# Kernel optimization log

Hardware: AMD Instinct MI355X
Metric: run time of the kernel (lower is better)

Reference implementation:

```python
import jax, jax.numpy as jnp
import numpy as np

LN_EPS = 1e-5


def setup_inputs() -> dict:
    key = jax.random.key(0)
    ks = jax.random.split(key, 6)
    N_NODES, N_EDGES, D, H, E = 100000, 20000, 128, 64, 1000000
    node_feat = jax.random.normal(ks[0], (N_NODES, D), dtype=jnp.float32)
    edge_feat = jax.random.normal(ks[1], (N_EDGES, D), dtype=jnp.float32)
    gamma = jnp.ones((2 * D,), dtype=jnp.float32)
    beta = jnp.zeros((2 * D,), dtype=jnp.float32)
    # xavier_uniform-like init
    lim1 = float(np.sqrt(6.0 / (2 * D + H)))
    lim2 = float(np.sqrt(6.0 / (H + 1)))
    W1 = jax.random.uniform(ks[2], (2 * D, H), minval=-lim1, maxval=lim1, dtype=jnp.float32)
    b1 = jnp.zeros((H,), dtype=jnp.float32)
    W2 = jax.random.uniform(ks[3], (H, 1), minval=-lim2, maxval=lim2, dtype=jnp.float32)
    b2 = jnp.zeros((1,), dtype=jnp.float32)
    node_idx = jax.random.randint(ks[4], (E,), 0, N_NODES, dtype=jnp.int64 if jax.config.read('jax_enable_x64') else jnp.int32)
    edge_idx = jax.random.randint(ks[5], (E,), 0, N_EDGES, dtype=node_idx.dtype)
    return {"node_feat": node_feat, "edge_feat": edge_feat, "gamma": gamma, "beta": beta,
            "W1": W1, "b1": b1, "W2": W2, "b2": b2,
            "node_idx": node_idx, "edge_idx": edge_idx}


def reference(node_feat, edge_feat, gamma, beta, W1, b1, W2, b2, node_idx, edge_idx):
    # Gather incidence-pair embeddings: [E, D] each
    emb_node = node_feat[node_idx]
    emb_edge = edge_feat[edge_idx]
    # combined: [E, 2D], order = [edge, node] as in torch.cat([emb_edge, emb_node], 1)
    combined = jnp.concatenate([emb_edge, emb_node], axis=1)
    # LayerNorm over last dim
    mu = jnp.mean(combined, axis=-1, keepdims=True)
    var = jnp.var(combined, axis=-1, keepdims=True)
    xn = (combined - mu) * jax.lax.rsqrt(var + LN_EPS) * gamma + beta
    # MLP: Linear -> ReLU -> Linear, output [E, 1]
    h = jax.nn.relu(xn @ W1 + b1)
    return h @ W2 + b2
```

## Files before the change

kernel.cpp:

```cpp
#include <hip/hip_runtime.h>

#define LN_EPS 1e-5f
#define DD 128
#define TWO_D 256
#define HH 64

typedef unsigned int uint;
typedef __attribute__((ext_vector_type(8))) short short8v;
typedef __attribute__((ext_vector_type(4))) float f32x4;

__device__ __forceinline__ unsigned short f2bf(float f) {
    uint u = __float_as_uint(f);
    u += 0x7FFFu + ((u >> 16) & 1u);
    return (unsigned short)(u >> 16);
}
__device__ __forceinline__ float bf2f(unsigned short h) {
    return __uint_as_float(((uint)h) << 16);
}

__global__ __launch_bounds__(256) void k_fused(
    const float* __restrict__ node_feat, int n_nodes, int nbN,
    const float* __restrict__ edge_feat, int n_edges,
    const float* __restrict__ gamma, const float* __restrict__ beta,
    const float* __restrict__ W1, const float* __restrict__ b1,
    unsigned short* __restrict__ node_pt, float2* __restrict__ node_sums,
    unsigned short* __restrict__ edge_pt, float2* __restrict__ edge_sums,
    float* __restrict__ GB) {
    int bid = blockIdx.x;
    int tid = threadIdx.x;

    if (bid == 0) {
        if (tid < 128) {
            int h = tid & 63;
            bool isB = tid >= 64;
            float acc = isB ? b1[h] : 0.f;
            const float* coef = isB ? beta : gamma;
#pragma unroll 8
            for (int d = 0; d < TWO_D; ++d)
                acc = fmaf(coef[d], W1[d * HH + h], acc);
            GB[tid] = acc;
        }
        return;
    }

    const float* feat;
    int nrows, gofs, rbase0;
    unsigned short* pt;
    float2* sums;
    if (bid <= nbN) {
        feat = node_feat; nrows = n_nodes; gofs = 128;
        rbase0 = (bid - 1) * 128; pt = node_pt; sums = node_sums;
    } else {
        feat = edge_feat; nrows = n_edges; gofs = 0;
        rbase0 = (bid - 1 - nbN) * 128; pt = edge_pt; sums = edge_sums;
    }

    __shared__ __align__(16) char lds[49152];

    {
        int l = tid & 63;
        int w = tid >> 6;
#pragma unroll
        for (int ci = 0; ci < 4; ++ci) {
            int combo = ci * 4 + w;
            int ks = combo & 3;
            int ht = combo >> 2;
            int kbase = gofs + ks * 32 + (l >> 4) * 8;
            int h = ht * 16 + (l & 15);
            unsigned short vals[8];
#pragma unroll
            for (int j = 0; j < 8; ++j)
                vals[j] = f2bf(gamma[kbase + j] * W1[(size_t)(kbase + j) * HH + h]);
            short8v v;
#pragma unroll
            for (int j = 0; j < 8; ++j) v[j] = (short)vals[j];
            *(short8v*)(lds + 32768 + combo * 1024 + l * 16) = v;
        }
    }

    {
        float4 tmp[16];
#pragma unroll
        for (int u = 0; u < 16; ++u) {
            int F4 = u * 256 + tid;
            int r = F4 >> 5;
            int rg = rbase0 + r;
            rg = rg < nrows ? rg : (nrows - 1);
            int c4 = (F4 & 31) * 4;
            tmp[u] = *(const float4*)&feat[(size_t)rg * DD + c4];
        }
#pragma unroll
        for (int u = 0; u < 16; ++u) {
            int F4 = u * 256 + tid;
            int r = F4 >> 5;
            int c4 = (F4 & 31) * 4;
            uint2 wv;
            wv.x = (uint)f2bf(tmp[u].x) | ((uint)f2bf(tmp[u].y) << 16);
            wv.y = (uint)f2bf(tmp[u].z) | ((uint)f2bf(tmp[u].w) << 16);
            int byte = (r * 256 + c4 * 2) ^ ((r & 7) << 4);
            *(uint2*)(lds + byte) = wv;
        }
    }

    __syncthreads();

    int w = tid >> 6;
    int lane = tid & 63;
    f32x4 acc[2][4];
#pragma unroll
    for (int i = 0; i < 2; ++i)
#pragma unroll
        for (int j = 0; j < 4; ++j) acc[i][j] = (f32x4){0.f, 0.f, 0.f, 0.f};

    int arow_lo = lane & 15;
    int akofs = (lane >> 4) * 8;
#pragma unroll
    for (int ks = 0; ks < 4; ++ks) {
        int kk = ks * 32 + akofs;
        int rr0 = (2 * w) * 16 + arow_lo;
        int rr1 = rr0 + 16;
        short8v a0 = *(const short8v*)(lds + ((rr0 * 256 + kk * 2) ^ ((rr0 & 7) << 4)));
        short8v a1 = *(const short8v*)(lds + ((rr1 * 256 + kk * 2) ^ ((rr1 & 7) << 4)));
#pragma unroll
        for (int ht = 0; ht < 4; ++ht) {
            short8v b = *(const short8v*)(lds + 32768 + (ht * 4 + ks) * 1024 + lane * 16);
            acc[0][ht] = __builtin_amdgcn_mfma_f32_16x16x32_bf16(a0, b, acc[0][ht], 0, 0, 0);
            acc[1][ht] = __builtin_amdgcn_mfma_f32_16x16x32_bf16(a1, b, acc[1][ht], 0, 0, 0);
        }
    }

    {
        int row = tid >> 1, half = tid & 1;
        float s = 0.f, q = 0.f;
#pragma unroll
        for (int i = 0; i < 8; ++i) {
            int byte = (row * 256 + half * 128 + i * 16) ^ ((row & 7) << 4);
            short8v v = *(const short8v*)(lds + byte);
#pragma unroll
            for (int j = 0; j < 8; ++j) {
                float x = bf2f((unsigned short)v[j]);
                s += x;
                q = fmaf(x, x, q);
            }
        }
        s += __shfl_xor(s, 1);
        q += __shfl_xor(q, 1);
        if (half == 0 && rbase0 + row < nrows) sums[rbase0 + row] = make_float2(s, q);
    }

    __syncthreads();

    {
        unsigned short* ob = (unsigned short*)(lds + 32768);
        int colh = lane & 15;
        int rquad = lane >> 4;
#pragma unroll
        for (int rt = 0; rt < 2; ++rt)
#pragma unroll
            for (int ht = 0; ht < 4; ++ht)
#pragma unroll
                for (int reg = 0; reg < 4; ++reg) {
                    int r = (2 * w + rt) * 16 + rquad * 4 + reg;
                    int h = ht * 16 + colh;
                    ob[r * 64 + h] = f2bf(acc[rt][ht][reg]);
                }
        int row = tid >> 1;
        if (rbase0 + row < nrows) {
#pragma unroll
            for (int i = 0; i < 4; ++i) {
                short8v v = *(const short8v*)(lds + 32768 + tid * 64 + i * 16);
                *(short8v*)&pt[(size_t)rbase0 * HH + tid * 32 + i * 8] = v;
            }
        }
    }
}

__global__ __launch_bounds__(256) void k_pairs(const int* __restrict__ node_idx,
                                               const int* __restrict__ edge_idx,
                                               const unsigned short* __restrict__ node_pt,
                                               const unsigned short* __restrict__ edge_pt,
                                               const float2* __restrict__ node_sums,
                                               const float2* __restrict__ edge_sums,
                                               const float* __restrict__ Gv,
                                               const float* __restrict__ Bv,
                                               const float* __restrict__ W2,
                                               const float* __restrict__ b2,
                                               float* __restrict__ out, int E) {
    int gtid = blockIdx.x * 256 + threadIdx.x;
    int l = gtid & 7;
    int grp = gtid >> 3;
    int ngrps = (gridDim.x * 256) >> 3;

    float G8[8], B8[8], W8[8];
#pragma unroll
    for (int j = 0; j < 8; ++j) {
        G8[j] = Gv[l * 8 + j];
        B8[j] = Bv[l * 8 + j];
        W8[j] = W2[l * 8 + j];
    }
    float b2v = b2[0];

#pragma unroll 2
    for (int p = grp; p < E; p += ngrps) {
        int ni = node_idx[p];
        int ei = edge_idx[p];
        uint4 ue = *(const uint4*)&edge_pt[(size_t)ei * HH + l * 8];
        uint4 un = *(const uint4*)&node_pt[(size_t)ni * HH + l * 8];
        float2 se = edge_sums[ei];
        float2 sn = node_sums[ni];

        float S = se.x + sn.x;
        float Q = se.y + sn.y;
        float mu = S * (1.f / TWO_D);
        float var = fmaf(Q, 1.f / TWO_D, -mu * mu);
        float rstd = rsqrtf(var + LN_EPS);
        float nmu = -mu;

        uint ue_[4] = {ue.x, ue.y, ue.z, ue.w};
        uint un_[4] = {un.x, un.y, un.z, un.w};
        float acc = 0.f;
#pragma unroll
        for (int j = 0; j < 4; ++j) {
            float pe0 = __uint_as_float(ue_[j] << 16);
            float pe1 = __uint_as_float(ue_[j] & 0xFFFF0000u);
            float pn0 = __uint_as_float(un_[j] << 16);
            float pn1 = __uint_as_float(un_[j] & 0xFFFF0000u);
            float t0 = fmaf(nmu, G8[2 * j], pe0 + pn0);
            float v0 = fmaf(rstd, t0, B8[2 * j]);
            v0 = fmaxf(v0, 0.f);
            acc = fmaf(v0, W8[2 * j], acc);
            float t1 = fmaf(nmu, G8[2 * j + 1], pe1 + pn1);
            float v1 = fmaf(rstd, t1, B8[2 * j + 1]);
            v1 = fmaxf(v1, 0.f);
            acc = fmaf(v1, W8[2 * j + 1], acc);
        }

        acc += __shfl_xor(acc, 1);
        acc += __shfl_xor(acc, 2);
        acc += __shfl_xor(acc, 4);

        if (l == 0) out[p] = acc + b2v;
    }
}

extern "C" void kernel_launch(void* const* d_in, const int* in_sizes, int n_in,
                              void* d_out, int out_size, void* d_ws, size_t ws_size,
                              hipStream_t stream) {
    const float* node_feat = (const float*)d_in[0];
    const float* edge_feat = (const float*)d_in[1];
    const float* gamma = (const float*)d_in[2];
    const float* beta = (const float*)d_in[3];
    const float* W1 = (const float*)d_in[4];
    const float* b1 = (const float*)d_in[5];
    const float* W2 = (const float*)d_in[6];
    const float* b2 = (const float*)d_in[7];
    const int* node_idx = (const int*)d_in[8];
    const int* edge_idx = (const int*)d_in[9];

    int n_nodes = in_sizes[0] / DD;
    int n_edges = in_sizes[1] / DD;
    int E = in_sizes[8];

    float* ws = (float*)d_ws;
    float* GB = ws;
    float2* node_sums = (float2*)(ws + 128);
    float2* edge_sums = node_sums + n_nodes;

    size_t off = 128 + 2 * (size_t)n_nodes + 2 * (size_t)n_edges;
    off = (off + 31) & ~(size_t)31;
    unsigned short* node_pt = (unsigned short*)(ws + off);
    unsigned short* edge_pt = node_pt + (size_t)n_nodes * HH;

    int nbN = (n_nodes + 127) / 128;
    int nbE = (n_edges + 127) / 128;

    k_fused<<<1 + nbN + nbE, 256, 0, stream>>>(node_feat, n_nodes, nbN,
                                               edge_feat, n_edges,
                                               gamma, beta, W1, b1,
                                               node_pt, node_sums,
                                               edge_pt, edge_sums, GB);
    k_pairs<<<2048, 256, 0, stream>>>(node_idx, edge_idx, node_pt, edge_pt,
                                      node_sums, edge_sums, GB, GB + 64, W2, b2,
                                      (float*)d_out, E);
}
```

Measured before the change: 55.08 us.

## Bin incidence pairs by node index range to improve gather locality

Adds a pre-pass that counts and scatters (node, edge, position) records into 8 buckets keyed by node-index range, then a pair kernel processes each bucket so concurrent blocks gather from a narrower slice of node projections. The aim is to raise L2 hit rate for the random bf16 node row gathers. It adds two extra launches, extra index read/write traffic and scattered output stores, and falls back to the old kernel when index ranges or workspace size don't fit the packing.

```diff
diff --git a/kernel.cpp b/kernel.cpp
--- a/kernel.cpp
+++ b/kernel.cpp
@@ -172,6 +172,115 @@
                 *(short8v*)&pt[(size_t)rbase0 * HH + tid * 32 + i * 8] = v;
             }
         }
+    }
+}
+
+__global__ void k_zero8(uint* gcnt) { gcnt[threadIdx.x] = 0; }
+
+__global__ __launch_bounds__(256) void k_bin(const int* __restrict__ node_idx,
+                                             const int* __restrict__ edge_idx,
+                                             int E, float scale, uint* __restrict__ gcnt,
+                                             uint2* __restrict__ binned, int Ecap) {
+    __shared__ uint lc[8];
+    __shared__ uint lofs[8];
+    int tid = threadIdx.x;
+    if (tid < 8) lc[tid] = 0;
+    __syncthreads();
+    int per = (E + (int)gridDim.x - 1) / (int)gridDim.x;
+    int s = blockIdx.x * per;
+    int e = s + per < E ? s + per : E;
+    for (int p = s + tid; p < e; p += 256) {
+        int b = (int)((float)node_idx[p] * scale);
+        b = b < 7 ? b : 7;
+        atomicAdd(&lc[b], 1u);
+    }
+    __syncthreads();
+    if (tid < 8) lofs[tid] = atomicAdd(&gcnt[tid], lc[tid]);
+    __syncthreads();
+    for (int p = s + tid; p < e; p += 256) {
+        int ni = node_idx[p];
+        int ei = edge_idx[p];
+        int b = (int)((float)ni * scale);
+        b = b < 7 ? b : 7;
+        uint pos = atomicAdd(&lofs[b], 1u);
+        binned[(size_t)b * Ecap + pos] = make_uint2((uint)ni | ((uint)ei << 17), (uint)p);
+    }
+}
+
+__global__ __launch_bounds__(256) void k_pairs_b(const uint2* __restrict__ binned, int Ecap,
+                                                 const uint* __restrict__ gcnt,
+                                                 const unsigned short* __restrict__ node_pt,
+                                                 const unsigned short* __restrict__ edge_pt,
+                                                 const float2* __restrict__ node_sums,
+                                                 const float2* __restrict__ edge_sums,
+                                                 const float* __restrict__ Gv,
+                                                 const float* __restrict__ Bv,
+                                                 const float* __restrict__ W2,
+                                                 const float* __restrict__ b2,
+                                                 float* __restrict__ out) {
+    int bucket = blockIdx.x & 7;
+    int nchunk = (int)gridDim.x >> 3;
+    int chunk = blockIdx.x >> 3;
+    uint sz = gcnt[bucket];
+    uint per = (sz + nchunk - 1) / nchunk;
+    uint beg = chunk * per;
+    uint end = beg + per < sz ? beg + per : sz;
+    const uint2* bb = binned + (size_t)bucket * Ecap;
+
+    int tid = threadIdx.x;
+    int l = tid & 7;
+    int grp = tid >> 3;
+
+    float G8[8], B8[8], W8[8];
+#pragma unroll
+    for (int j = 0; j < 8; ++j) {
+        G8[j] = Gv[l * 8 + j];
+        B8[j] = Bv[l * 8 + j];
+        W8[j] = W2[l * 8 + j];
+    }
+    float b2v = b2[0];
+
+#pragma unroll 2
+    for (uint i = beg + grp; i < end; i += 32) {
+        uint2 rec = bb[i];
+        uint ni = rec.x & 0x1FFFFu;
+        uint ei = rec.x >> 17;
+        uint4 ue = *(const uint4*)&edge_pt[(size_t)ei * HH + l * 8];
+        uint4 un = *(const uint4*)&node_pt[(size_t)ni * HH + l * 8];
+        float2 se = edge_sums[ei];
+        float2 sn = node_sums[ni];
+
+        float S = se.x + sn.x;
+        float Q = se.y + sn.y;
+        float mu = S * (1.f / TWO_D);
+        float var = fmaf(Q, 1.f / TWO_D, -mu * mu);
+        float rstd = rsqrtf(var + LN_EPS);
+        float nmu = -mu;
+
+        uint ue_[4] = {ue.x, ue.y, ue.z, ue.w};
+        uint un_[4] = {un.x, un.y, un.z, un.w};
+        float acc = 0.f;
+#pragma unroll
+        for (int j = 0; j < 4; ++j) {
+            float pe0 = __uint_as_float(ue_[j] << 16);
+            float pe1 = __uint_as_float(ue_[j] & 0xFFFF0000u);
+            float pn0 = __uint_as_float(un_[j] << 16);
+            float pn1 = __uint_as_float(un_[j] & 0xFFFF0000u);
+            float t0 = fmaf(nmu, G8[2 * j], pe0 + pn0);
+            float v0 = fmaf(rstd, t0, B8[2 * j]);
+            v0 = fmaxf(v0, 0.f);
+            acc = fmaf(v0, W8[2 * j], acc);
+            float t1 = fmaf(nmu, G8[2 * j + 1], pe1 + pn1);
+            float v1 = fmaf(rstd, t1, B8[2 * j + 1]);
+            v1 = fmaxf(v1, 0.f);
+            acc = fmaf(v1, W8[2 * j + 1], acc);
+        }
+
+        acc += __shfl_xor(acc, 1);
+        acc += __shfl_xor(acc, 2);
+        acc += __shfl_xor(acc, 4);
+
+        if (l == 0) out[rec.y] = acc + b2v;
     }
 }
 
@@ -261,25 +370,43 @@
     int n_edges = in_sizes[1] / DD;
     int E = in_sizes[8];
 
-    float* ws = (float*)d_ws;
-    float* GB = ws;
-    float2* node_sums = (float2*)(ws + 128);
-    float2* edge_sums = node_sums + n_nodes;
-
-    size_t off = 128 + 2 * (size_t)n_nodes + 2 * (size_t)n_edges;
-    off = (off + 31) & ~(size_t)31;
-    unsigned short* node_pt = (unsigned short*)(ws + off);
-    unsigned short* edge_pt = node_pt + (size_t)n_nodes * HH;
+    char* wsb = (char*)d_ws;
+    size_t o = 0;
+    float* GB = (float*)(wsb + o); o += 512;
+    float2* node_sums = (float2*)(wsb + o); o += (size_t)n_nodes * 8;
+    float2* edge_sums = (float2*)(wsb + o); o += (size_t)n_edges * 8;
+    o = (o + 127) & ~(size_t)127;
+    unsigned short* node_pt = (unsigned short*)(wsb + o); o += (size_t)n_nodes * HH * 2;
+    unsigned short* edge_pt = (unsigned short*)(wsb + o); o += (size_t)n_edges * HH * 2;
+    o = (o + 127) & ~(size_t)127;
+    uint* gcnt = (uint*)(wsb + o); o += 128;
+    uint2* binned = (uint2*)(wsb + o);
+    size_t need = o + (size_t)8 * (size_t)E * sizeof(uint2);
+
+    bool can_bin = (n_nodes <= (1 << 17)) && (n_edges <= (1 << 15)) && (ws_size >= need);
 
     int nbN = (n_nodes + 127) / 128;
     int nbE = (n_edges + 127) / 128;
+
+    if (can_bin) {
+        float scale = 8.0f / (float)n_nodes;
+        k_zero8<<<1, 8, 0, stream>>>(gcnt);
+        k_bin<<<256, 256, 0, stream>>>(node_idx, edge_idx, E, scale, gcnt, binned, E);
+    }
 
     k_fused<<<1 + nbN + nbE, 256, 0, stream>>>(node_feat, n_nodes, nbN,
                                                edge_feat, n_edges,
                                                gamma, beta, W1, b1,
                                                node_pt, node_sums,
                                                edge_pt, edge_sums, GB);
-    k_pairs<<<2048, 256, 0, stream>>>(node_idx, edge_idx, node_pt, edge_pt,
-                                      node_sums, edge_sums, GB, GB + 64, W2, b2,
-                                      (float*)d_out, E);
-}
+
+    if (can_bin) {
+        k_pairs_b<<<2048, 256, 0, stream>>>(binned, E, gcnt, node_pt, edge_pt,
+                                            node_sums, edge_sums, GB, GB + 64, W2, b2,
+                                            (float*)d_out);
+    } else {
+        k_pairs<<<2048, 256, 0, stream>>>(node_idx, edge_idx, node_pt, edge_pt,
+                                          node_sums, edge_sums, GB, GB + 64, W2, b2,
+                                          (float*)d_out, E);
+    }
+}
```

Measured after the change: 73.01 us. 32.5% more time.

## Quantize per-row projected features to int8 with per-row scales

Applied to the files above, without the earlier changes.

The per-row partial projections (64 values per node or edge row) are now stored as int8 with a per-row absmax scale instead of bf16. The scale is packed with the LayerNorm sums into a float4. This halves the bytes gathered per incidence pair in the random-access pairs kernel, and the stores now write directly from the MFMA accumulator layout using a permuted hidden index. The costs are added quantization error (int8 with per-row scale) and a 16-byte rather than 8-byte stats load per row. The loop unroll also rises from 2 to 4.

```diff
diff --git a/kernel.cpp b/kernel.cpp
--- a/kernel.cpp
+++ b/kernel.cpp
@@ -23,8 +23,8 @@
     const float* __restrict__ edge_feat, int n_edges,
     const float* __restrict__ gamma, const float* __restrict__ beta,
     const float* __restrict__ W1, const float* __restrict__ b1,
-    unsigned short* __restrict__ node_pt, float2* __restrict__ node_sums,
-    unsigned short* __restrict__ edge_pt, float2* __restrict__ edge_sums,
+    signed char* __restrict__ node_pt, float4* __restrict__ node_st,
+    signed char* __restrict__ edge_pt, float4* __restrict__ edge_st,
     float* __restrict__ GB) {
     int bid = blockIdx.x;
     int tid = threadIdx.x;
@@ -45,17 +45,18 @@
 
     const float* feat;
     int nrows, gofs, rbase0;
-    unsigned short* pt;
-    float2* sums;
+    signed char* pt;
+    float4* st;
     if (bid <= nbN) {
         feat = node_feat; nrows = n_nodes; gofs = 128;
-        rbase0 = (bid - 1) * 128; pt = node_pt; sums = node_sums;
+        rbase0 = (bid - 1) * 128; pt = node_pt; st = node_st;
     } else {
         feat = edge_feat; nrows = n_edges; gofs = 0;
-        rbase0 = (bid - 1 - nbN) * 128; pt = edge_pt; sums = edge_sums;
-    }
-
-    __shared__ __align__(16) char lds[49152];
+        rbase0 = (bid - 1 - nbN) * 128; pt = edge_pt; st = edge_st;
+    }
+
+    __shared__ __align__(16) char lds[49664];
+    float* scaleLDS = (float*)(lds + 49152);
 
     {
         int l = tid & 63;
@@ -67,13 +68,10 @@
             int ht = combo >> 2;
             int kbase = gofs + ks * 32 + (l >> 4) * 8;
             int h = ht * 16 + (l & 15);
-            unsigned short vals[8];
+            short8v v;
 #pragma unroll
             for (int j = 0; j < 8; ++j)
-                vals[j] = f2bf(gamma[kbase + j] * W1[(size_t)(kbase + j) * HH + h]);
-            short8v v;
-#pragma unroll
-            for (int j = 0; j < 8; ++j) v[j] = (short)vals[j];
+                v[j] = (short)f2bf(gamma[kbase + j] * W1[(size_t)(kbase + j) * HH + h]);
             *(short8v*)(lds + 32768 + combo * 1024 + l * 16) = v;
         }
     }
@@ -130,6 +128,36 @@
     }
 
     {
+        int colh = lane & 15;
+        int rquad = lane >> 4;
+#pragma unroll
+        for (int rt = 0; rt < 2; ++rt)
+#pragma unroll
+            for (int reg = 0; reg < 4; ++reg) {
+                float m = fmaxf(fmaxf(fabsf(acc[rt][0][reg]), fabsf(acc[rt][1][reg])),
+                                fmaxf(fabsf(acc[rt][2][reg]), fabsf(acc[rt][3][reg])));
+                m = fmaxf(m, __shfl_xor(m, 1));
+                m = fmaxf(m, __shfl_xor(m, 2));
+                m = fmaxf(m, __shfl_xor(m, 4));
+                m = fmaxf(m, __shfl_xor(m, 8));
+                m = fmaxf(m, 1e-20f);
+                float inv = 127.0f / m;
+                uint pk = 0;
+#pragma unroll
+                for (int ht = 0; ht < 4; ++ht) {
+                    int q = __float2int_rn(acc[rt][ht][reg] * inv);
+                    pk |= ((uint)q & 0xFFu) << (8 * ht);
+                }
+                int rl = (2 * w + rt) * 16 + rquad * 4 + reg;
+                if (rbase0 + rl < nrows)
+                    *(uint*)&pt[(size_t)(rbase0 + rl) * 64 + colh * 4] = pk;
+                if (colh == 0) scaleLDS[rl] = m * (1.0f / 127.0f);
+            }
+    }
+
+    __syncthreads();
+
+    {
         int row = tid >> 1, half = tid & 1;
         float s = 0.f, q = 0.f;
 #pragma unroll
@@ -145,42 +173,17 @@
         }
         s += __shfl_xor(s, 1);
         q += __shfl_xor(q, 1);
-        if (half == 0 && rbase0 + row < nrows) sums[rbase0 + row] = make_float2(s, q);
-    }
-
-    __syncthreads();
-
-    {
-        unsigned short* ob = (unsigned short*)(lds + 32768);
-        int colh = lane & 15;
-        int rquad = lane >> 4;
-#pragma unroll
-        for (int rt = 0; rt < 2; ++rt)
-#pragma unroll
-            for (int ht = 0; ht < 4; ++ht)
-#pragma unroll
-                for (int reg = 0; reg < 4; ++reg) {
-                    int r = (2 * w + rt) * 16 + rquad * 4 + reg;
-                    int h = ht * 16 + colh;
-                    ob[r * 64 + h] = f2bf(acc[rt][ht][reg]);
-                }
-        int row = tid >> 1;
-        if (rbase0 + row < nrows) {
-#pragma unroll
-            for (int i = 0; i < 4; ++i) {
-                short8v v = *(const short8v*)(lds + 32768 + tid * 64 + i * 16);
-                *(short8v*)&pt[(size_t)rbase0 * HH + tid * 32 + i * 8] = v;
-            }
-        }
+        if (half == 0 && rbase0 + row < nrows)
+            st[rbase0 + row] = make_float4(s, q, scaleLDS[row], 0.f);
     }
 }
 
 __global__ __launch_bounds__(256) void k_pairs(const int* __restrict__ node_idx,
                                                const int* __restrict__ edge_idx,
-                                               const unsigned short* __restrict__ node_pt,
-                                               const unsigned short* __restrict__ edge_pt,
-                                               const float2* __restrict__ node_sums,
-                                               const float2* __restrict__ edge_sums,
+                                               const signed char* __restrict__ node_pt,
+                                               const signed char* __restrict__ edge_pt,
+                                               const float4* __restrict__ node_st,
+                                               const float4* __restrict__ edge_st,
                                                const float* __restrict__ Gv,
                                                const float* __restrict__ Bv,
                                                const float* __restrict__ W2,
@@ -194,20 +197,22 @@
     float G8[8], B8[8], W8[8];
 #pragma unroll
     for (int j = 0; j < 8; ++j) {
-        G8[j] = Gv[l * 8 + j];
-        B8[j] = Bv[l * 8 + j];
-        W8[j] = W2[l * 8 + j];
+        int k = l * 8 + j;
+        int h = (k & 3) * 16 + (k >> 2);
+        G8[j] = Gv[h];
+        B8[j] = Bv[h];
+        W8[j] = W2[h];
     }
     float b2v = b2[0];
 
-#pragma unroll 2
+#pragma unroll 4
     for (int p = grp; p < E; p += ngrps) {
         int ni = node_idx[p];
         int ei = edge_idx[p];
-        uint4 ue = *(const uint4*)&edge_pt[(size_t)ei * HH + l * 8];
-        uint4 un = *(const uint4*)&node_pt[(size_t)ni * HH + l * 8];
-        float2 se = edge_sums[ei];
-        float2 sn = node_sums[ni];
+        uint2 qe2 = *(const uint2*)&edge_pt[(size_t)ei * 64 + l * 8];
+        uint2 qn2 = *(const uint2*)&node_pt[(size_t)ni * 64 + l * 8];
+        float4 se = edge_st[ei];
+        float4 sn = node_st[ni];
 
         float S = se.x + sn.x;
         float Q = se.y + sn.y;
@@ -215,24 +220,20 @@
         float var = fmaf(Q, 1.f / TWO_D, -mu * mu);
         float rstd = rsqrtf(var + LN_EPS);
         float nmu = -mu;
-
-        uint ue_[4] = {ue.x, ue.y, ue.z, ue.w};
-        uint un_[4] = {un.x, un.y, un.z, un.w};
+        float esc = se.z, nsc = sn.z;
+
         float acc = 0.f;
 #pragma unroll
-        for (int j = 0; j < 4; ++j) {
-            float pe0 = __uint_as_float(ue_[j] << 16);
-            float pe1 = __uint_as_float(ue_[j] & 0xFFFF0000u);
-            float pn0 = __uint_as_float(un_[j] << 16);
-            float pn1 = __uint_as_float(un_[j] & 0xFFFF0000u);
-            float t0 = fmaf(nmu, G8[2 * j], pe0 + pn0);
-            float v0 = fmaf(rstd, t0, B8[2 * j]);
-            v0 = fmaxf(v0, 0.f);
-            acc = fmaf(v0, W8[2 * j], acc);
-            float t1 = fmaf(nmu, G8[2 * j + 1], pe1 + pn1);
-            float v1 = fmaf(rstd, t1, B8[2 * j + 1]);
-            v1 = fmaxf(v1, 0.f);
-            acc = fmaf(v1, W8[2 * j + 1], acc);
+        for (int j = 0; j < 8; ++j) {
+            uint we = (j < 4) ? qe2.x : qe2.y;
+            uint wn = (j < 4) ? qn2.x : qn2.y;
+            int qa = (int)(signed char)(we >> (8 * (j & 3)));
+            int qb = (int)(signed char)(wn >> (8 * (j & 3)));
+            float v = fmaf((float)qa, esc, (float)qb * nsc);
+            float t = fmaf(nmu, G8[j], v);
+            float hv = fmaf(rstd, t, B8[j]);
+            hv = fmaxf(hv, 0.f);
+            acc = fmaf(hv, W8[j], acc);
         }
 
         acc += __shfl_xor(acc, 1);
@@ -261,15 +262,14 @@
     int n_edges = in_sizes[1] / DD;
     int E = in_sizes[8];
 
-    float* ws = (float*)d_ws;
-    float* GB = ws;
-    float2* node_sums = (float2*)(ws + 128);
-    float2* edge_sums = node_sums + n_nodes;
-
-    size_t off = 128 + 2 * (size_t)n_nodes + 2 * (size_t)n_edges;
-    off = (off + 31) & ~(size_t)31;
-    unsigned short* node_pt = (unsigned short*)(ws + off);
-    unsigned short* edge_pt = node_pt + (size_t)n_nodes * HH;
+    char* wsb = (char*)d_ws;
+    size_t o = 0;
+    float* GB = (float*)(wsb + o); o += 512;
+    float4* node_st = (float4*)(wsb + o); o += (size_t)n_nodes * 16;
+    float4* edge_st = (float4*)(wsb + o); o += (size_t)n_edges * 16;
+    o = (o + 127) & ~(size_t)127;
+    signed char* node_pt = (signed char*)(wsb + o); o += (size_t)n_nodes * 64;
+    signed char* edge_pt = (signed char*)(wsb + o); o += (size_t)n_edges * 64;
 
     int nbN = (n_nodes + 127) / 128;
     int nbE = (n_edges + 127) / 128;
@@ -277,9 +277,9 @@
     k_fused<<<1 + nbN + nbE, 256, 0, stream>>>(node_feat, n_nodes, nbN,
                                                edge_feat, n_edges,
                                                gamma, beta, W1, b1,
-                                               node_pt, node_sums,
-                                               edge_pt, edge_sums, GB);
+                                               node_pt, node_st,
+                                               edge_pt, edge_st, GB);
     k_pairs<<<2048, 256, 0, stream>>>(node_idx, edge_idx, node_pt, edge_pt,
-                                      node_sums, edge_sums, GB, GB + 64, W2, b2,
+                                      node_st, edge_st, GB, GB + 64, W2, b2,
                                       (float*)d_out, E);
 }
```

Result: no change. 54.36 us (-1.3%).
